# Kernel optimization log

Measured on AMD Instinct MI355X. Metric: run time of the kernel, lower is better.

## Reference

```python
import jax, jax.numpy as jnp
import numpy as np

N_NODES = 500000
HID = 128
N_EDGES = 1000000


def setup_inputs() -> dict:
    key = jax.random.key(0)
    k1, k2, k3, k4 = jax.random.split(key, 4)
    z_author = jax.random.normal(k1, (N_NODES, HID), dtype=jnp.float32)
    edge_label_index = jax.random.randint(k2, (2, N_EDGES), 0, N_NODES, dtype=jnp.int64)
    # torch Linear default init scale ~ 1/sqrt(fan_in); exact values irrelevant for correctness baseline
    W1 = jax.random.normal(k3, (2 * HID, HID), dtype=jnp.float32) / np.sqrt(2 * HID)
    b1 = jnp.zeros((HID,), dtype=jnp.float32)
    W2 = jax.random.normal(k4, (HID, 1), dtype=jnp.float32) / np.sqrt(HID)
    b2 = jnp.zeros((1,), dtype=jnp.float32)
    return {"z_author": z_author, "edge_label_index": edge_label_index,
            "W1": W1, "b1": b1, "W2": W2, "b2": b2}


def reference(z_author, edge_label_index, W1, b1, W2, b2):
    row, col = edge_label_index[0], edge_label_index[1]
    # gather rows + concat -> [E, 2*HID]
    z = jnp.concatenate([z_author[row], z_author[col]], axis=-1)
    z = jax.nn.relu(z @ W1 + b1)   # [E, HID]
    z = z @ W2 + b2                # [E, 1]
    return z.reshape(-1)
```

## Files before the change

kernel.cpp:

```cpp
#include <hip/hip_runtime.h>
#include <stdint.h>

#define HID 128

typedef __bf16 bf16x8 __attribute__((ext_vector_type(8)));
typedef float f32x4 __attribute__((ext_vector_type(4)));

__device__ __forceinline__ unsigned short f2bf(float x) {
  unsigned int u = __float_as_uint(x);
  u += 0x7fffu + ((u >> 16) & 1u);
  return (unsigned short)(u >> 16);
}

__global__ void cvt_z_kernel(const float* __restrict__ z,
                             unsigned short* __restrict__ zb, long n8) {
  long i = (long)blockIdx.x * blockDim.x + threadIdx.x;
  const long stride = (long)gridDim.x * blockDim.x;
  const float4* zf = (const float4*)z;
  uint4* o = (uint4*)zb;
  for (; i < n8; i += stride) {
    float4 v0 = zf[2 * i];
    float4 v1 = zf[2 * i + 1];
    uint4 w;
    w.x = f2bf(v0.x) | ((unsigned)f2bf(v0.y) << 16);
    w.y = f2bf(v0.z) | ((unsigned)f2bf(v0.w) << 16);
    w.z = f2bf(v1.x) | ((unsigned)f2bf(v1.y) << 16);
    w.w = f2bf(v1.z) | ((unsigned)f2bf(v1.w) << 16);
    o[i] = w;
  }
}

__global__ void cvt_w1_kernel(const float* __restrict__ W1,
                              unsigned short* __restrict__ w1t) {
  int idx = blockIdx.x * blockDim.x + threadIdx.x;
  if (idx < 256 * HID) {
    int k = idx >> 7, n = idx & 127;
    w1t[n * 256 + (k ^ ((n & 7) << 3))] = f2bf(W1[idx]);
  }
}

template <bool ZB>
__global__ __launch_bounds__(512, 4) void edge_mlp_kernel(
    const float* __restrict__ zf, const unsigned short* __restrict__ zb,
    const int* __restrict__ eli, const unsigned short* __restrict__ w1t,
    const float* __restrict__ b1, const float* __restrict__ W2,
    const float* __restrict__ b2, float* __restrict__ out, int nE) {
  __shared__ __align__(16) unsigned short wt[128 * 256];
  const int tid = threadIdx.x;
  {
    const uint4* g = (const uint4*)w1t;
    uint4* s = (uint4*)wt;
#pragma unroll
    for (int j = 0; j < 8; ++j) s[tid + j * 512] = g[tid + j * 512];
  }
  __syncthreads();

  const int lane = tid & 63;
  const int wid = tid >> 6;
  const int l15 = lane & 15;
  const int l4 = lane >> 4;
  const int koff = l4 * 8;
  const int xorv = (lane & 7) << 3;

  const int ebase = blockIdx.x * 256 + wid * 32;

  const int e0 = ebase + l15;
  const int e1 = ebase + 16 + l15;
  const int e0c = e0 < nE ? e0 : 0;
  const int e1c = e1 < nE ? e1 : 0;
  const int r0 = eli[e0c], c0 = eli[nE + e0c];
  const int r1 = eli[e1c], c1 = eli[nE + e1c];

  f32x4 acc[2][8] = {};

#pragma unroll
  for (int ks = 0; ks < 8; ++ks) {
    const int half = ks >> 2;
    const int kk = (ks & 3) * 32 + koff;
    bf16x8 a0, a1;
    if (ZB) {
      a0 = __builtin_bit_cast(bf16x8, *(const uint4*)(zb + (long)(half ? c0 : r0) * HID + kk));
      a1 = __builtin_bit_cast(bf16x8, *(const uint4*)(zb + (long)(half ? c1 : r1) * HID + kk));
    } else {
      const float* p0 = zf + (long)(half ? c0 : r0) * HID + kk;
      const float* p1 = zf + (long)(half ? c1 : r1) * HID + kk;
      float4 u0 = *(const float4*)p0, u1 = *(const float4*)(p0 + 4);
      float4 v0 = *(const float4*)p1, v1 = *(const float4*)(p1 + 4);
      uint4 wa, wb;
      wa.x = f2bf(u0.x) | ((unsigned)f2bf(u0.y) << 16);
      wa.y = f2bf(u0.z) | ((unsigned)f2bf(u0.w) << 16);
      wa.z = f2bf(u1.x) | ((unsigned)f2bf(u1.y) << 16);
      wa.w = f2bf(u1.z) | ((unsigned)f2bf(u1.w) << 16);
      wb.x = f2bf(v0.x) | ((unsigned)f2bf(v0.y) << 16);
      wb.y = f2bf(v0.z) | ((unsigned)f2bf(v0.w) << 16);
      wb.z = f2bf(v1.x) | ((unsigned)f2bf(v1.y) << 16);
      wb.w = f2bf(v1.z) | ((unsigned)f2bf(v1.w) << 16);
      a0 = __builtin_bit_cast(bf16x8, wa);
      a1 = __builtin_bit_cast(bf16x8, wb);
    }
    const int klog = ks * 32 + koff;
#pragma unroll
    for (int nf = 0; nf < 8; ++nf) {
      const int n = nf * 16 + l15;
      const bf16x8 b = __builtin_bit_cast(
          bf16x8, *(const uint4*)&wt[n * 256 + (klog ^ xorv)]);
      acc[0][nf] = __builtin_amdgcn_mfma_f32_16x16x32_bf16(a0, b, acc[0][nf], 0, 0, 0);
      acc[1][nf] = __builtin_amdgcn_mfma_f32_16x16x32_bf16(a1, b, acc[1][nf], 0, 0, 0);
    }
  }

  float b1v[8], w2v[8];
#pragma unroll
  for (int nf = 0; nf < 8; ++nf) {
    b1v[nf] = b1[nf * 16 + l15];
    w2v[nf] = W2[nf * 16 + l15];
  }
  const float bias2 = b2[0];

#pragma unroll
  for (int mg = 0; mg < 2; ++mg) {
    float p0 = 0.f, p1 = 0.f, p2 = 0.f, p3 = 0.f;
#pragma unroll
    for (int nf = 0; nf < 8; ++nf) {
      f32x4 h = acc[mg][nf];
      float t;
      t = h[0] + b1v[nf]; p0 += (t > 0.f ? t : 0.f) * w2v[nf];
      t = h[1] + b1v[nf]; p1 += (t > 0.f ? t : 0.f) * w2v[nf];
      t = h[2] + b1v[nf]; p2 += (t > 0.f ? t : 0.f) * w2v[nf];
      t = h[3] + b1v[nf]; p3 += (t > 0.f ? t : 0.f) * w2v[nf];
    }
#pragma unroll
    for (int off = 1; off < 16; off <<= 1) {
      p0 += __shfl_xor(p0, off);
      p1 += __shfl_xor(p1, off);
      p2 += __shfl_xor(p2, off);
      p3 += __shfl_xor(p3, off);
    }
    if (l15 == 0) {
      const int m0 = ebase + mg * 16 + l4 * 4;
      if (m0 + 0 < nE) out[m0 + 0] = p0 + bias2;
      if (m0 + 1 < nE) out[m0 + 1] = p1 + bias2;
      if (m0 + 2 < nE) out[m0 + 2] = p2 + bias2;
      if (m0 + 3 < nE) out[m0 + 3] = p3 + bias2;
    }
  }
}

__global__ void naive_kernel(const float* __restrict__ z, const int* __restrict__ eli,
                             const float* __restrict__ W1, const float* __restrict__ b1,
                             const float* __restrict__ W2, const float* __restrict__ b2,
                             float* __restrict__ out, int nE) {
  int e = blockIdx.x * blockDim.x + threadIdx.x;
  if (e >= nE) return;
  const float* zr = z + (long)eli[e] * HID;
  const float* zc = z + (long)eli[nE + e] * HID;
  float s = b2[0];
  for (int n = 0; n < HID; ++n) {
    float h = b1[n];
    for (int k = 0; k < HID; ++k)
      h += zr[k] * W1[k * HID + n] + zc[k] * W1[(k + HID) * HID + n];
    s += (h > 0.f ? h : 0.f) * W2[n];
  }
  out[e] = s;
}

extern "C" void kernel_launch(void* const* d_in, const int* in_sizes, int n_in,
                              void* d_out, int out_size, void* d_ws, size_t ws_size,
                              hipStream_t stream) {
  const float* z = (const float*)d_in[0];
  const int* eli = (const int*)d_in[1];
  const float* W1 = (const float*)d_in[2];
  const float* b1 = (const float*)d_in[3];
  const float* W2 = (const float*)d_in[4];
  const float* b2 = (const float*)d_in[5];
  float* out = (float*)d_out;

  const int nE = out_size;
  const long nZ = in_sizes[0];
  const size_t W1T_BYTES = 256 * HID * sizeof(unsigned short);
  const size_t ZB_BYTES = (size_t)nZ * 2;

  if (ws_size < W1T_BYTES) {
    naive_kernel<<<(nE + 255) / 256, 256, 0, stream>>>(z, eli, W1, b1, W2, b2, out, nE);
    return;
  }

  unsigned short* w1t = (unsigned short*)d_ws;
  unsigned short* zb = (unsigned short*)((char*)d_ws + W1T_BYTES);
  const bool use_zb = ws_size >= W1T_BYTES + ZB_BYTES;

  cvt_w1_kernel<<<(256 * HID + 255) / 256, 256, 0, stream>>>(W1, w1t);
  if (use_zb) cvt_z_kernel<<<2048, 256, 0, stream>>>(z, zb, nZ / 8);

  const int nblocks = (nE + 255) / 256;
  if (use_zb)
    edge_mlp_kernel<true><<<nblocks, 512, 0, stream>>>(z, zb, eli, w1t, b1, W2, b2, out, nE);
  else
    edge_mlp_kernel<false><<<nblocks, 512, 0, stream>>>(z, zb, eli, w1t, b1, W2, b2, out, nE);
}
```

Measured before the change: 175.1 us.

## Stage gathered bf16 rows into LDS via async global_load_lds and halve edges per block

Gathered bf16 embedding rows are now copied straight into a per-wave swizzled LDS staging buffer with global_load_lds. The MFMA loop starts on the row half while the column half is still loading, split by vmcnt waits. Each wave now handles 16 edges instead of 32, so each W1 LDS fragment is reused half as often. Occupancy drops to 2 blocks per CU, LDS use per block roughly doubles, and the fp32 fallback path is removed.

Measured after the change: 218.9 us. +25.0%, slower.

```diff
diff --git a/kernel.cpp b/kernel.cpp
--- a/kernel.cpp
+++ b/kernel.cpp
@@ -39,13 +39,19 @@
   }
 }
 
-template <bool ZB>
-__global__ __launch_bounds__(512, 4) void edge_mlp_kernel(
-    const float* __restrict__ zf, const unsigned short* __restrict__ zb,
-    const int* __restrict__ eli, const unsigned short* __restrict__ w1t,
-    const float* __restrict__ b1, const float* __restrict__ W2,
-    const float* __restrict__ b2, float* __restrict__ out, int nE) {
+__device__ __forceinline__ void gload_lds16(const void* g, void* l) {
+  __builtin_amdgcn_global_load_lds(
+      (const __attribute__((address_space(1))) unsigned int*)g,
+      (__attribute__((address_space(3))) unsigned int*)l, 16, 0, 0);
+}
+
+__global__ __launch_bounds__(512, 2) void edge_mlp_kernel(
+    const unsigned short* __restrict__ zb, const int* __restrict__ eli,
+    const unsigned short* __restrict__ w1t, const float* __restrict__ b1,
+    const float* __restrict__ W2, const float* __restrict__ b2,
+    float* __restrict__ out, int nE) {
   __shared__ __align__(16) unsigned short wt[128 * 256];
+  __shared__ __align__(16) unsigned char stage[8 * 8192];
   const int tid = threadIdx.x;
   {
     const uint4* g = (const uint4*)w1t;
@@ -62,50 +68,57 @@
   const int koff = l4 * 8;
   const int xorv = (lane & 7) << 3;
 
-  const int ebase = blockIdx.x * 256 + wid * 32;
-
-  const int e0 = ebase + l15;
-  const int e1 = ebase + 16 + l15;
-  const int e0c = e0 < nE ? e0 : 0;
-  const int e1c = e1 < nE ? e1 : 0;
-  const int r0 = eli[e0c], c0 = eli[nE + e0c];
-  const int r1 = eli[e1c], c1 = eli[nE + e1c];
-
-  f32x4 acc[2][8] = {};
-
-#pragma unroll
-  for (int ks = 0; ks < 8; ++ks) {
-    const int half = ks >> 2;
-    const int kk = (ks & 3) * 32 + koff;
-    bf16x8 a0, a1;
-    if (ZB) {
-      a0 = __builtin_bit_cast(bf16x8, *(const uint4*)(zb + (long)(half ? c0 : r0) * HID + kk));
-      a1 = __builtin_bit_cast(bf16x8, *(const uint4*)(zb + (long)(half ? c1 : r1) * HID + kk));
-    } else {
-      const float* p0 = zf + (long)(half ? c0 : r0) * HID + kk;
-      const float* p1 = zf + (long)(half ? c1 : r1) * HID + kk;
-      float4 u0 = *(const float4*)p0, u1 = *(const float4*)(p0 + 4);
-      float4 v0 = *(const float4*)p1, v1 = *(const float4*)(p1 + 4);
-      uint4 wa, wb;
-      wa.x = f2bf(u0.x) | ((unsigned)f2bf(u0.y) << 16);
-      wa.y = f2bf(u0.z) | ((unsigned)f2bf(u0.w) << 16);
-      wa.z = f2bf(u1.x) | ((unsigned)f2bf(u1.y) << 16);
-      wa.w = f2bf(u1.z) | ((unsigned)f2bf(u1.w) << 16);
-      wb.x = f2bf(v0.x) | ((unsigned)f2bf(v0.y) << 16);
-      wb.y = f2bf(v0.z) | ((unsigned)f2bf(v0.w) << 16);
-      wb.z = f2bf(v1.x) | ((unsigned)f2bf(v1.y) << 16);
-      wb.w = f2bf(v1.z) | ((unsigned)f2bf(v1.w) << 16);
-      a0 = __builtin_bit_cast(bf16x8, wa);
-      a1 = __builtin_bit_cast(bf16x8, wb);
-    }
+  const int ebase = blockIdx.x * 128 + wid * 16;
+  unsigned char* sw = stage + wid * 8192;
+
+  const int j3 = lane >> 3;
+  const int s8 = lane & 7;
+#pragma unroll
+  for (int g = 0; g < 4; ++g) {
+    const int rl = g * 8 + j3;
+    const int e = ebase + (rl & 15);
+    const int ec = e < nE ? e : 0;
+    const int nid = (rl < 16) ? eli[ec] : eli[nE + ec];
+    const char* gb = (const char*)zb + (long)nid * 256 + ((s8 ^ (rl & 7)) * 16);
+    gload_lds16(gb, sw + g * 1024);
+    gload_lds16(gb + 128, sw + 4096 + g * 1024);
+  }
+
+  f32x4 acc[8] = {};
+
+  asm volatile("s_waitcnt vmcnt(4)" ::: "memory");
+  __builtin_amdgcn_sched_barrier(0);
+#pragma unroll
+  for (int ks = 0; ks < 4; ++ks) {
+    const int h2 = (ks >> 1) & 1;
+    const int slot = (((ks & 1) * 4 + l4) ^ (l15 & 7));
+    const bf16x8 a = __builtin_bit_cast(
+        bf16x8, *(const uint4*)(sw + h2 * 4096 + l15 * 128 + slot * 16));
     const int klog = ks * 32 + koff;
 #pragma unroll
     for (int nf = 0; nf < 8; ++nf) {
       const int n = nf * 16 + l15;
       const bf16x8 b = __builtin_bit_cast(
           bf16x8, *(const uint4*)&wt[n * 256 + (klog ^ xorv)]);
-      acc[0][nf] = __builtin_amdgcn_mfma_f32_16x16x32_bf16(a0, b, acc[0][nf], 0, 0, 0);
-      acc[1][nf] = __builtin_amdgcn_mfma_f32_16x16x32_bf16(a1, b, acc[1][nf], 0, 0, 0);
+      acc[nf] = __builtin_amdgcn_mfma_f32_16x16x32_bf16(a, b, acc[nf], 0, 0, 0);
+    }
+  }
+
+  asm volatile("s_waitcnt vmcnt(0)" ::: "memory");
+  __builtin_amdgcn_sched_barrier(0);
+#pragma unroll
+  for (int ks = 4; ks < 8; ++ks) {
+    const int h2 = (ks >> 1) & 1;
+    const int slot = (((ks & 1) * 4 + l4) ^ (l15 & 7));
+    const bf16x8 a = __builtin_bit_cast(
+        bf16x8, *(const uint4*)(sw + h2 * 4096 + (16 + l15) * 128 + slot * 16));
+    const int klog = ks * 32 + koff;
+#pragma unroll
+    for (int nf = 0; nf < 8; ++nf) {
+      const int n = nf * 16 + l15;
+      const bf16x8 b = __builtin_bit_cast(
+          bf16x8, *(const uint4*)&wt[n * 256 + (klog ^ xorv)]);
+      acc[nf] = __builtin_amdgcn_mfma_f32_16x16x32_bf16(a, b, acc[nf], 0, 0, 0);
     }
   }
 
@@ -117,32 +130,29 @@
   }
   const float bias2 = b2[0];
 
-#pragma unroll
-  for (int mg = 0; mg < 2; ++mg) {
-    float p0 = 0.f, p1 = 0.f, p2 = 0.f, p3 = 0.f;
-#pragma unroll
-    for (int nf = 0; nf < 8; ++nf) {
-      f32x4 h = acc[mg][nf];
-      float t;
-      t = h[0] + b1v[nf]; p0 += (t > 0.f ? t : 0.f) * w2v[nf];
-      t = h[1] + b1v[nf]; p1 += (t > 0.f ? t : 0.f) * w2v[nf];
-      t = h[2] + b1v[nf]; p2 += (t > 0.f ? t : 0.f) * w2v[nf];
-      t = h[3] + b1v[nf]; p3 += (t > 0.f ? t : 0.f) * w2v[nf];
-    }
-#pragma unroll
-    for (int off = 1; off < 16; off <<= 1) {
-      p0 += __shfl_xor(p0, off);
-      p1 += __shfl_xor(p1, off);
-      p2 += __shfl_xor(p2, off);
-      p3 += __shfl_xor(p3, off);
-    }
-    if (l15 == 0) {
-      const int m0 = ebase + mg * 16 + l4 * 4;
-      if (m0 + 0 < nE) out[m0 + 0] = p0 + bias2;
-      if (m0 + 1 < nE) out[m0 + 1] = p1 + bias2;
-      if (m0 + 2 < nE) out[m0 + 2] = p2 + bias2;
-      if (m0 + 3 < nE) out[m0 + 3] = p3 + bias2;
-    }
+  float p0 = 0.f, p1 = 0.f, p2 = 0.f, p3 = 0.f;
+#pragma unroll
+  for (int nf = 0; nf < 8; ++nf) {
+    f32x4 h = acc[nf];
+    float t;
+    t = h[0] + b1v[nf]; p0 += (t > 0.f ? t : 0.f) * w2v[nf];
+    t = h[1] + b1v[nf]; p1 += (t > 0.f ? t : 0.f) * w2v[nf];
+    t = h[2] + b1v[nf]; p2 += (t > 0.f ? t : 0.f) * w2v[nf];
+    t = h[3] + b1v[nf]; p3 += (t > 0.f ? t : 0.f) * w2v[nf];
+  }
+#pragma unroll
+  for (int off = 1; off < 16; off <<= 1) {
+    p0 += __shfl_xor(p0, off);
+    p1 += __shfl_xor(p1, off);
+    p2 += __shfl_xor(p2, off);
+    p3 += __shfl_xor(p3, off);
+  }
+  if (l15 == 0) {
+    const int m0 = ebase + l4 * 4;
+    if (m0 + 0 < nE) out[m0 + 0] = p0 + bias2;
+    if (m0 + 1 < nE) out[m0 + 1] = p1 + bias2;
+    if (m0 + 2 < nE) out[m0 + 2] = p2 + bias2;
+    if (m0 + 3 < nE) out[m0 + 3] = p3 + bias2;
   }
 }
 
@@ -180,21 +190,17 @@
   const size_t W1T_BYTES = 256 * HID * sizeof(unsigned short);
   const size_t ZB_BYTES = (size_t)nZ * 2;
 
-  if (ws_size < W1T_BYTES) {
+  if (ws_size < W1T_BYTES + ZB_BYTES) {
     naive_kernel<<<(nE + 255) / 256, 256, 0, stream>>>(z, eli, W1, b1, W2, b2, out, nE);
     return;
   }
 
   unsigned short* w1t = (unsigned short*)d_ws;
   unsigned short* zb = (unsigned short*)((char*)d_ws + W1T_BYTES);
-  const bool use_zb = ws_size >= W1T_BYTES + ZB_BYTES;
 
   cvt_w1_kernel<<<(256 * HID + 255) / 256, 256, 0, stream>>>(W1, w1t);
-  if (use_zb) cvt_z_kernel<<<2048, 256, 0, stream>>>(z, zb, nZ / 8);
-
-  const int nblocks = (nE + 255) / 256;
-  if (use_zb)
-    edge_mlp_kernel<true><<<nblocks, 512, 0, stream>>>(z, zb, eli, w1t, b1, W2, b2, out, nE);
-  else
-    edge_mlp_kernel<false><<<nblocks, 512, 0, stream>>>(z, zb, eli, w1t, b1, W2, b2, out, nE);
-}
+  cvt_z_kernel<<<2048, 256, 0, stream>>>(z, zb, nZ / 8);
+
+  const int nblocks = (nE + 127) / 128;
+  edge_mlp_kernel<<<nblocks, 512, 0, stream>>>(zb, eli, w1t, b1, W2, b2, out, nE);
+}
```
